# Kernel tuning notes

Measured on AMD Instinct MI355X. Metric: run time of the kernel, lower is better.

The kernel has to match this reference:

```python
import jax, jax.numpy as jnp
import numpy as np

N = 100_000   # num nodes
E = 1_000_000 # num edges
F = 64        # feat_dim
H = 64        # hidden_dim
D = 64        # embed_dim


def _xavier(key, shape):
    limit = float(np.sqrt(6.0 / (shape[0] + shape[1])))
    return jax.random.uniform(key, shape, jnp.float32, -limit, limit)


def setup_inputs() -> dict:
    key = jax.random.key(0)
    ks = jax.random.split(key, 8)
    x = jax.random.normal(ks[0], (N, F), jnp.float32)
    edge_index = jax.random.randint(ks[1], (2, E), 0, N, dtype=jnp.int64)
    # GCNConv weights stored [in, out] (torch Linear transposed); biases zero-init
    return {
        "x": x,
        "edge_index": edge_index,
        "W1": _xavier(ks[2], (F, H)), "b1": jnp.zeros((H,), jnp.float32),
        "W2": _xavier(ks[3], (H, H)), "b2": jnp.zeros((H,), jnp.float32),
        "W3": _xavier(ks[4], (H, D)), "b3": jnp.zeros((D,), jnp.float32),
        "fw1": _xavier(ks[5], (D, H)), "fb1": jnp.zeros((H,), jnp.float32),
        "fw2": _xavier(ks[6], (H, D)), "fb2": jnp.zeros((D,), jnp.float32),
    }


def _gcn_conv(x, src, dst, dinv, W, b):
    # GCNConv: out = D^{-1/2} (A+I) D^{-1/2} (x W) + b
    h = x @ W                                   # [N, out]
    norm = dinv[src] * dinv[dst]                # [E]
    msg = h[src] * norm[:, None]                # gather + scale: [E, out]
    agg = jax.ops.segment_sum(msg, dst, num_segments=N)
    agg = agg + h * (dinv * dinv)[:, None]      # self-loop term
    return agg + b


def reference(x, edge_index, W1, b1, W2, b2, W3, b3, fw1, fb1, fw2, fb2):
    src, dst = edge_index[0], edge_index[1]
    # degree with self-loops (symmetric normalization)
    deg = jax.ops.segment_sum(jnp.ones((E,), x.dtype), dst, num_segments=N) + 1.0
    dinv = jax.lax.rsqrt(deg)
    # eval mode: dropout(p=0.5, training=False) is identity
    h = jax.nn.relu(_gcn_conv(x, src, dst, dinv, W1, b1))
    h = jax.nn.relu(_gcn_conv(h, src, dst, dinv, W2, b2))
    h = jax.nn.relu(_gcn_conv(h, src, dst, dinv, W3, b3))
    h = jax.nn.relu(h @ fw1 + fb1)
    return h @ fw2 + fb2                        # node embeddings [N, D]
```

## Files before the change

### kernel.cpp

```cpp
#include <hip/hip_runtime.h>
#include <cstdint>
#include <cstddef>


#define CDIV(a, b) (((a) + (b) - 1) / (b))

typedef __attribute__((ext_vector_type(8))) short bf16x8;
typedef __attribute__((ext_vector_type(4))) float f32x4;

static constexpr int BKT_SHIFT = 10;
static constexpr int BKT_NODES = 1 << BKT_SHIFT;
static constexpr int BKT_CAP = 13312;

__device__ __forceinline__ void split_bf(float a, short& hi, short& lo) {
  unsigned u = __float_as_uint(a);
  unsigned r = u + (0x7FFF + ((u >> 16) & 1));
  hi = (short)(r >> 16);
  float hirec = __uint_as_float(r & 0xFFFF0000u);
  float res = a - hirec;
  lo = (short)(__float_as_uint(res) >> 16);
}

__device__ __forceinline__ unsigned short f2bf_rne(float a) {
  unsigned u = __float_as_uint(a);
  u += 0x7FFF + ((u >> 16) & 1);
  return (unsigned short)(u >> 16);
}

__device__ __forceinline__ float4 bf4_to_f4(uint2 u) {
  float4 v;
  v.x = __uint_as_float(u.x << 16);
  v.y = __uint_as_float(u.x & 0xFFFF0000u);
  v.z = __uint_as_float(u.y << 16);
  v.w = __uint_as_float(u.y & 0xFFFF0000u);
  return v;
}

__device__ __forceinline__ void split8(float4 x, float4 y, bf16x8& h, bf16x8& l) {
  float av[8] = {x.x, x.y, x.z, x.w, y.x, y.y, y.z, y.w};
#pragma unroll
  for (int j = 0; j < 8; ++j) {
    short hi, lo;
    split_bf(av[j], hi, lo);
    h[j] = hi;
    l[j] = lo;
  }
}

__device__ __forceinline__ float4 nt_ld4(const float* p) {
  f32x4 v = __builtin_nontemporal_load(reinterpret_cast<const f32x4*>(p));
  float4 r;
  r.x = v[0]; r.y = v[1]; r.z = v[2]; r.w = v[3];
  return r;
}

__global__ void k_zero_i32(int* __restrict__ p, int n) {
  int i = blockIdx.x * blockDim.x + threadIdx.x;
  if (i < n) p[i] = 0;
}

__global__ __launch_bounds__(256)
void k_bucket(const int* __restrict__ ei, int* __restrict__ bcnt,
              int2* __restrict__ pairs, int E) {
  __shared__ int hist[128], rbase[128], roff[128];
  int t = threadIdx.x;
  int chunk = (E + gridDim.x - 1) / gridDim.x;
  int e0 = blockIdx.x * chunk;
  int e1 = min(e0 + chunk, E);
  if (t < 128) hist[t] = 0;
  __syncthreads();
  for (int e = e0 + t; e < e1; e += 256) {
    int d = __builtin_nontemporal_load(&ei[E + e]);
    atomicAdd(&hist[d >> BKT_SHIFT], 1);
  }
  __syncthreads();
  if (t < 128) {
    roff[t] = 0;
    rbase[t] = hist[t] ? atomicAdd(&bcnt[t], hist[t]) : 0;
  }
  __syncthreads();
  for (int e = e0 + t; e < e1; e += 256) {
    int d = __builtin_nontemporal_load(&ei[E + e]);
    int s = __builtin_nontemporal_load(&ei[e]);
    int b = d >> BKT_SHIFT;
    int r = atomicAdd(&roff[b], 1);
    int idx = rbase[b] + r;
    if (idx < BKT_CAP) pairs[(size_t)b * BKT_CAP + idx] = make_int2(s, d);
  }
}

__global__ __launch_bounds__(1024)
void k_build(const int2* __restrict__ pairs, const int* __restrict__ bcnt,
             int* __restrict__ row_ptr, float* __restrict__ dinv,
             int* __restrict__ srcs, int N, int E, int K) {
  __shared__ int cnt[BKT_NODES];
  __shared__ int deg[BKT_NODES];
  __shared__ int ebase_sh;
  int b = blockIdx.x;
  int t = threadIdx.x;
  int lo = b << BKT_SHIFT;
  int range = min(BKT_NODES, N - lo);
  int sz = min(bcnt[b], BKT_CAP);
  if (t == 0) {
    int s = 0;
    for (int i = 0; i < b; ++i) s += bcnt[i];
    ebase_sh = s;
  }
  cnt[t] = 0;
  __syncthreads();
  int ebase = ebase_sh;
  const int2* pb = pairs + (size_t)b * BKT_CAP;
  for (int i = t; i < sz; i += 1024) {
    atomicAdd(&cnt[pb[i].y - lo], 1);
  }
  __syncthreads();
  deg[t] = cnt[t];
  __syncthreads();
  int offset = 1;
  for (int d2 = BKT_NODES / 2; d2 > 0; d2 >>= 1) {
    if (t < d2) {
      int ai = offset * (2 * t + 1) - 1;
      int bi = offset * (2 * t + 2) - 1;
      cnt[bi] += cnt[ai];
    }
    offset <<= 1;
    __syncthreads();
  }
  if (t == 0) cnt[BKT_NODES - 1] = 0;
  __syncthreads();
  for (int d2 = 1; d2 < BKT_NODES; d2 <<= 1) {
    offset >>= 1;
    if (t < d2) {
      int ai = offset * (2 * t + 1) - 1;
      int bi = offset * (2 * t + 2) - 1;
      int tmp = cnt[ai];
      cnt[ai] = cnt[bi];
      cnt[bi] += tmp;
    }
    __syncthreads();
  }
  if (t < range) {
    row_ptr[lo + t] = ebase + cnt[t];
    dinv[lo + t] = rsqrtf((float)deg[t] + 1.0f);
  }
  if (b == K - 1 && t == 0) row_ptr[N] = E;
  __syncthreads();
  for (int i = t; i < sz; i += 1024) {
    int2 p = pb[i];
    int pos = ebase + atomicAdd(&cnt[p.y - lo], 1);
    srcs[pos] = p.x;
  }
}

__global__ void k_prep(const float* __restrict__ w0, const float* __restrict__ w1,
                       const float* __restrict__ w2, const float* __restrict__ w3,
                       const float* __restrict__ w4, bf16x8* __restrict__ packed) {
  const float* W;
  switch (blockIdx.x) {
    case 0: W = w0; break;
    case 1: W = w1; break;
    case 2: W = w2; break;
    case 3: W = w3; break;
    default: W = w4; break;
  }
  int tid = threadIdx.x;
  int lane = tid & 63;
  int q = (tid >> 6) & 1;
  int t = tid >> 7;
  int col = lane & 15, quad = lane >> 4;
  bf16x8 hi8, lo8;
#pragma unroll
  for (int j = 0; j < 8; ++j) {
    int k = q * 32 + quad * 8 + j;
    short hi, lo;
    split_bf(W[k * 64 + t * 16 + col], hi, lo);
    hi8[j] = hi;
    lo8[j] = lo;
  }
  size_t base = (size_t)blockIdx.x * 1024 + ((t * 2 + q) * 2) * 64 + lane;
  packed[base] = hi8;
  packed[base + 64] = lo8;
}

__global__ __launch_bounds__(256, 4)
void k_mm(const float* __restrict__ in, const bf16x8* __restrict__ Wp,
          const float* __restrict__ dinv, unsigned short* __restrict__ out, int n) {
  int lane = threadIdx.x & 63;
  int col = lane & 15, quad = lane >> 4;
  int tile = (blockIdx.x * blockDim.x + threadIdx.x) >> 6;
  int ntiles = (n + 15) >> 4;
  if (tile >= ntiles) return;

  bf16x8 wh[4][2], wl[4][2];
#pragma unroll
  for (int t = 0; t < 4; ++t)
#pragma unroll
    for (int q = 0; q < 2; ++q) {
      wh[t][q] = Wp[((t * 2 + q) * 2) * 64 + lane];
      wl[t][q] = Wp[((t * 2 + q) * 2 + 1) * 64 + lane];
    }

  int row0 = tile << 4;
  int ar = row0 + col;
  if (ar > n - 1) ar = n - 1;
  const float* arow = in + (size_t)ar * 64 + quad * 8;
  float4 a0 = nt_ld4(arow), a1 = nt_ld4(arow + 4);
  float4 a2 = nt_ld4(arow + 32), a3 = nt_ld4(arow + 36);

  bf16x8 ah[2], al[2];
  split8(a0, a1, ah[0], al[0]);
  split8(a2, a3, ah[1], al[1]);

  f32x4 acc[4];
#pragma unroll
  for (int t = 0; t < 4; ++t) acc[t] = (f32x4){0.f, 0.f, 0.f, 0.f};
#pragma unroll
  for (int t = 0; t < 4; ++t)
#pragma unroll
    for (int q = 0; q < 2; ++q) {
      acc[t] = __builtin_amdgcn_mfma_f32_16x16x32_bf16(ah[q], wh[t][q], acc[t], 0, 0, 0);
      acc[t] = __builtin_amdgcn_mfma_f32_16x16x32_bf16(ah[q], wl[t][q], acc[t], 0, 0, 0);
      acc[t] = __builtin_amdgcn_mfma_f32_16x16x32_bf16(al[q], wh[t][q], acc[t], 0, 0, 0);
    }
  float dv[4];
#pragma unroll
  for (int r = 0; r < 4; ++r) {
    int row = row0 + quad * 4 + r;
    dv[r] = (row < n) ? dinv[row] : 0.0f;
  }
#pragma unroll
  for (int t = 0; t < 4; ++t)
#pragma unroll
    for (int r = 0; r < 4; ++r) {
      int row = row0 + quad * 4 + r;
      if (row < n) out[(size_t)row * 64 + t * 16 + col] = f2bf_rne(acc[t][r] * dv[r]);
    }
}

template <bool HEAD>
__global__ __launch_bounds__(256, 4)
void k_agg_mm(const unsigned short* __restrict__ hws, const float* __restrict__ dinv,
              const int* __restrict__ row_ptr, const int* __restrict__ srcs,
              const float* __restrict__ bagg,
              const bf16x8* __restrict__ Wp1, const float* __restrict__ b1p,
              const bf16x8* __restrict__ Wp2, const float* __restrict__ b2p,
              void* __restrict__ out, int n) {
  constexpr int LDP = 68;
  __shared__ float a_sh[16 * LDP];
  int tid = threadIdx.x;
  int g = tid >> 4;
  int fg = tid & 15;
  int row0 = blockIdx.x << 4;
  const uint2* hw2 = (const uint2*)hws;

  int node = row0 + g;
  bool valid = node < n;
  int nd = valid ? node : (n - 1);
  uint2 su = hw2[(size_t)nd * 16 + fg];
  int p0 = 0, p1 = 0;
  if (valid) {
    p0 = row_ptr[node];
    p1 = row_ptr[node + 1];
  }
  float4 acc = make_float4(0.f, 0.f, 0.f, 0.f);
  if (p0 < p1) {
    int s[8];
#pragma unroll
    for (int j = 0; j < 8; ++j) {
      int ij = p0 + j;
      ij = (ij < p1) ? ij : (p1 - 1);
      s[j] = __builtin_nontemporal_load(&srcs[ij]);
    }
    for (int p = p0; p < p1; p += 8) {
      uint2 u[8];
#pragma unroll
      for (int j = 0; j < 8; ++j) u[j] = hw2[(size_t)s[j] * 16 + fg];
      int pn = p + 8;
      if (pn < p1) {
#pragma unroll
        for (int j = 0; j < 8; ++j) {
          int ij = pn + j;
          ij = (ij < p1) ? ij : (p1 - 1);
          s[j] = __builtin_nontemporal_load(&srcs[ij]);
        }
      }
      float4 v0 = bf4_to_f4(u[0]);
      acc.x += v0.x;
      acc.y += v0.y;
      acc.z += v0.z;
      acc.w += v0.w;
#pragma unroll
      for (int j = 1; j < 8; ++j) {
        float m = (p + j < p1) ? 1.f : 0.f;
        float4 v = bf4_to_f4(u[j]);
        acc.x = fmaf(m, v.x, acc.x);
        acc.y = fmaf(m, v.y, acc.y);
        acc.z = fmaf(m, v.z, acc.z);
        acc.w = fmaf(m, v.w, acc.w);
      }
    }
  }
  {
    float di = valid ? dinv[node] : 0.f;
    float4 selfv = bf4_to_f4(su);
    float4 b4 = ((const float4*)bagg)[fg];
    float4 r = make_float4(0.f, 0.f, 0.f, 0.f);
    if (valid) {
      r.x = fmaxf(fmaf(di, acc.x + selfv.x, b4.x), 0.f);
      r.y = fmaxf(fmaf(di, acc.y + selfv.y, b4.y), 0.f);
      r.z = fmaxf(fmaf(di, acc.z + selfv.z, b4.z), 0.f);
      r.w = fmaxf(fmaf(di, acc.w + selfv.w, b4.w), 0.f);
    }
    *(float4*)&a_sh[g * LDP + (fg << 2)] = r;
  }
  __syncthreads();

  int lane = threadIdx.x & 63;
  int wave = threadIdx.x >> 6;
  int col = lane & 15, quad = lane >> 4;
  const float* arow = &a_sh[col * LDP + (quad << 3)];
  float4 a0 = *(const float4*)(arow);
  float4 a1 = *(const float4*)(arow + 4);
  float4 a2 = *(const float4*)(arow + 32);
  float4 a3 = *(const float4*)(arow + 36);
  bf16x8 ah[2], al[2];
  split8(a0, a1, ah[0], al[0]);
  split8(a2, a3, ah[1], al[1]);

  bf16x8 wh[2], wl[2];
#pragma unroll
  for (int q = 0; q < 2; ++q) {
    wh[q] = Wp1[((wave * 2 + q) * 2) * 64 + lane];
    wl[q] = Wp1[((wave * 2 + q) * 2 + 1) * 64 + lane];
  }
  f32x4 acc1 = (f32x4){0.f, 0.f, 0.f, 0.f};
#pragma unroll
  for (int q = 0; q < 2; ++q) {
    acc1 = __builtin_amdgcn_mfma_f32_16x16x32_bf16(ah[q], wh[q], acc1, 0, 0, 0);
    acc1 = __builtin_amdgcn_mfma_f32_16x16x32_bf16(ah[q], wl[q], acc1, 0, 0, 0);
    acc1 = __builtin_amdgcn_mfma_f32_16x16x32_bf16(al[q], wh[q], acc1, 0, 0, 0);
  }

  if constexpr (!HEAD) {
#pragma unroll
    for (int r = 0; r < 4; ++r) {
      int row = row0 + (quad << 2) + r;
      if (row < n) {
        ((unsigned short*)out)[(size_t)row * 64 + wave * 16 + col] =
            f2bf_rne(acc1[r] * dinv[row]);
      }
    }
  } else {
    __shared__ float h_sh[16 * LDP];
    float bv1 = b1p[wave * 16 + col];
#pragma unroll
    for (int r = 0; r < 4; ++r) {
      h_sh[((quad << 2) + r) * LDP + wave * 16 + col] = fmaxf(acc1[r] + bv1, 0.f);
    }
    __syncthreads();
    const float* hrow = &h_sh[col * LDP + (quad << 3)];
    float4 h0 = *(const float4*)(hrow);
    float4 h1 = *(const float4*)(hrow + 4);
    float4 h2 = *(const float4*)(hrow + 32);
    float4 h3 = *(const float4*)(hrow + 36);
    bf16x8 ah2[2], al2[2];
    split8(h0, h1, ah2[0], al2[0]);
    split8(h2, h3, ah2[1], al2[1]);
    bf16x8 wh2[2], wl2[2];
#pragma unroll
    for (int q = 0; q < 2; ++q) {
      wh2[q] = Wp2[((wave * 2 + q) * 2) * 64 + lane];
      wl2[q] = Wp2[((wave * 2 + q) * 2 + 1) * 64 + lane];
    }
    f32x4 acc2 = (f32x4){0.f, 0.f, 0.f, 0.f};
#pragma unroll
    for (int q = 0; q < 2; ++q) {
      acc2 = __builtin_amdgcn_mfma_f32_16x16x32_bf16(ah2[q], wh2[q], acc2, 0, 0, 0);
      acc2 = __builtin_amdgcn_mfma_f32_16x16x32_bf16(ah2[q], wl2[q], acc2, 0, 0, 0);
      acc2 = __builtin_amdgcn_mfma_f32_16x16x32_bf16(al2[q], wh2[q], acc2, 0, 0, 0);
    }
    float bv2 = b2p[wave * 16 + col];
#pragma unroll
    for (int r = 0; r < 4; ++r) {
      int row = row0 + (quad << 2) + r;
      if (row < n) {
        ((float*)out)[(size_t)row * 64 + wave * 16 + col] = acc2[r] + bv2;
      }
    }
  }
}

extern "C" void kernel_launch(void* const* d_in, const int* in_sizes, int n_in,
                              void* d_out, int out_size, void* d_ws, size_t ws_size,
                              hipStream_t stream) {
  const float* x = (const float*)d_in[0];
  const int* ei = (const int*)d_in[1];
  const float* W1 = (const float*)d_in[2];
  const float* b1 = (const float*)d_in[3];
  const float* W2 = (const float*)d_in[4];
  const float* b2 = (const float*)d_in[5];
  const float* W3 = (const float*)d_in[6];
  const float* b3 = (const float*)d_in[7];
  const float* fw1 = (const float*)d_in[8];
  const float* fb1 = (const float*)d_in[9];
  const float* fw2 = (const float*)d_in[10];
  const float* fb2 = (const float*)d_in[11];
  float* out = (float*)d_out;

  const int N = in_sizes[0] / 64;
  const int E = in_sizes[1] / 2;
  const int K = CDIV(N, BKT_NODES);

  char* w = (char*)d_ws;
  auto take = [&](size_t bytes) -> char* {
    char* p = w;
    w += (bytes + 255) & ~(size_t)255;
    return p;
  };
  float* dinv = (float*)take((size_t)N * 4);
  int* row_ptr = (int*)take((size_t)(N + 1) * 4);
  int* bcnt = (int*)take((size_t)128 * 4);
  int* srcs = (int*)take((size_t)E * 4);
  bf16x8* wpack = (bf16x8*)take((size_t)5 * 1024 * 16);
  unsigned short* hwsA = (unsigned short*)take((size_t)N * 64 * 2);
  unsigned short* hwsB = (unsigned short*)take((size_t)N * 64 * 2);
  int2* pairs = (int2*)hwsA;

  const int B = 256;

  k_prep<<<5, 512, 0, stream>>>(W1, W2, W3, fw1, fw2, wpack);
  k_zero_i32<<<1, 128, 0, stream>>>(bcnt, 128);
  k_bucket<<<256, B, 0, stream>>>(ei, bcnt, pairs, E);
  k_build<<<K, 1024, 0, stream>>>(pairs, bcnt, row_ptr, dinv, srcs, N, E, K);

  const int ntiles = CDIV(N, 16);
  const int MMG = CDIV(ntiles, 4);

  k_mm<<<MMG, B, 0, stream>>>(x, wpack + 0 * 1024, dinv, hwsA, N);
  k_agg_mm<false><<<ntiles, B, 0, stream>>>(hwsA, dinv, row_ptr, srcs, b1,
                                            wpack + 1 * 1024, nullptr, nullptr, nullptr,
                                            hwsB, N);
  k_agg_mm<false><<<ntiles, B, 0, stream>>>(hwsB, dinv, row_ptr, srcs, b2,
                                            wpack + 2 * 1024, nullptr, nullptr, nullptr,
                                            hwsA, N);
  k_agg_mm<true><<<ntiles, B, 0, stream>>>(hwsA, dinv, row_ptr, srcs, b3,
                                           wpack + 3 * 1024, fb1, wpack + 4 * 1024, fb2,
                                           out, N);
}
```

Baseline: 255.7 us.

## Widen gather to 16B per lane, 32 nodes per block, zero-row padding

The aggregation kernel now uses 8 lanes per node, each loading a 16-byte chunk of 8 bf16 features, and handles 32 nodes per block with two MFMA row tiles. Padded edge slots point at an extra all-zero row N instead of being masked by multiplication. The producing kernels write that zero row. Separately, the bucket-counter zeroing is folded into the weight-prep kernel to drop one launch, and the bucket grid grows to 1024 blocks. The aim is fewer, wider gather loads and less per-edge masking math, at the cost of more registers per thread and extra workspace for the padded row.

Result: slower. 271.2 us (+6.1%).

```diff
diff --git a/kernel.cpp b/kernel.cpp
--- a/kernel.cpp
+++ b/kernel.cpp
@@ -27,15 +27,6 @@
   return (unsigned short)(u >> 16);
 }
 
-__device__ __forceinline__ float4 bf4_to_f4(uint2 u) {
-  float4 v;
-  v.x = __uint_as_float(u.x << 16);
-  v.y = __uint_as_float(u.x & 0xFFFF0000u);
-  v.z = __uint_as_float(u.y << 16);
-  v.w = __uint_as_float(u.y & 0xFFFF0000u);
-  return v;
-}
-
 __device__ __forceinline__ void split8(float4 x, float4 y, bf16x8& h, bf16x8& l) {
   float av[8] = {x.x, x.y, x.z, x.w, y.x, y.y, y.z, y.w};
 #pragma unroll
@@ -52,11 +43,6 @@
   float4 r;
   r.x = v[0]; r.y = v[1]; r.z = v[2]; r.w = v[3];
   return r;
-}
-
-__global__ void k_zero_i32(int* __restrict__ p, int n) {
-  int i = blockIdx.x * blockDim.x + threadIdx.x;
-  if (i < n) p[i] = 0;
 }
 
 __global__ __launch_bounds__(256)
@@ -154,7 +140,12 @@
 
 __global__ void k_prep(const float* __restrict__ w0, const float* __restrict__ w1,
                        const float* __restrict__ w2, const float* __restrict__ w3,
-                       const float* __restrict__ w4, bf16x8* __restrict__ packed) {
+                       const float* __restrict__ w4, bf16x8* __restrict__ packed,
+                       int* __restrict__ bcnt) {
+  if (blockIdx.x == 5) {
+    if (threadIdx.x < 128) bcnt[threadIdx.x] = 0;
+    return;
+  }
   const float* W;
   switch (blockIdx.x) {
     case 0: W = w0; break;
@@ -185,6 +176,9 @@
 __global__ __launch_bounds__(256, 4)
 void k_mm(const float* __restrict__ in, const bf16x8* __restrict__ Wp,
           const float* __restrict__ dinv, unsigned short* __restrict__ out, int n) {
+  if (blockIdx.x == 0 && threadIdx.x < 32) {
+    ((unsigned int*)out)[(size_t)n * 32 + threadIdx.x] = 0u;
+  }
   int lane = threadIdx.x & 63;
   int col = lane & 15, quad = lane >> 4;
   int tile = (blockIdx.x * blockDim.x + threadIdx.x) >> 6;
@@ -246,86 +240,89 @@
               const bf16x8* __restrict__ Wp2, const float* __restrict__ b2p,
               void* __restrict__ out, int n) {
   constexpr int LDP = 68;
-  __shared__ float a_sh[16 * LDP];
+  __shared__ float a_sh[32 * LDP];
   int tid = threadIdx.x;
-  int g = tid >> 4;
-  int fg = tid & 15;
-  int row0 = blockIdx.x << 4;
-  const uint2* hw2 = (const uint2*)hws;
+  int g = tid >> 3;
+  int fg = tid & 7;
+  int row0 = blockIdx.x << 5;
+  const uint4* hw4 = (const uint4*)hws;
+
+  if (!HEAD && blockIdx.x == 0 && tid < 32) {
+    ((unsigned int*)out)[(size_t)n * 32 + tid] = 0u;
+  }
 
   int node = row0 + g;
   bool valid = node < n;
-  int nd = valid ? node : (n - 1);
-  uint2 su = hw2[(size_t)nd * 16 + fg];
+  int nd = valid ? node : n;
+  uint4 su = hw4[(size_t)nd * 8 + fg];
+  float di = valid ? dinv[node] : 0.f;
   int p0 = 0, p1 = 0;
   if (valid) {
     p0 = row_ptr[node];
     p1 = row_ptr[node + 1];
   }
-  float4 acc = make_float4(0.f, 0.f, 0.f, 0.f);
+  float acc[8] = {0.f, 0.f, 0.f, 0.f, 0.f, 0.f, 0.f, 0.f};
   if (p0 < p1) {
     int s[8];
 #pragma unroll
     for (int j = 0; j < 8; ++j) {
       int ij = p0 + j;
-      ij = (ij < p1) ? ij : (p1 - 1);
-      s[j] = __builtin_nontemporal_load(&srcs[ij]);
+      bool ok = ij < p1;
+      int sv = __builtin_nontemporal_load(&srcs[ok ? ij : p1 - 1]);
+      s[j] = ok ? sv : n;
     }
     for (int p = p0; p < p1; p += 8) {
-      uint2 u[8];
-#pragma unroll
-      for (int j = 0; j < 8; ++j) u[j] = hw2[(size_t)s[j] * 16 + fg];
+      uint4 u[8];
+#pragma unroll
+      for (int j = 0; j < 8; ++j) u[j] = hw4[(size_t)s[j] * 8 + fg];
       int pn = p + 8;
       if (pn < p1) {
 #pragma unroll
         for (int j = 0; j < 8; ++j) {
           int ij = pn + j;
-          ij = (ij < p1) ? ij : (p1 - 1);
-          s[j] = __builtin_nontemporal_load(&srcs[ij]);
+          bool ok = ij < p1;
+          int sv = __builtin_nontemporal_load(&srcs[ok ? ij : p1 - 1]);
+          s[j] = ok ? sv : n;
         }
       }
-      float4 v0 = bf4_to_f4(u[0]);
-      acc.x += v0.x;
-      acc.y += v0.y;
-      acc.z += v0.z;
-      acc.w += v0.w;
-#pragma unroll
-      for (int j = 1; j < 8; ++j) {
-        float m = (p + j < p1) ? 1.f : 0.f;
-        float4 v = bf4_to_f4(u[j]);
-        acc.x = fmaf(m, v.x, acc.x);
-        acc.y = fmaf(m, v.y, acc.y);
-        acc.z = fmaf(m, v.z, acc.z);
-        acc.w = fmaf(m, v.w, acc.w);
+#pragma unroll
+      for (int j = 0; j < 8; ++j) {
+        acc[0] += __uint_as_float(u[j].x << 16);
+        acc[1] += __uint_as_float(u[j].x & 0xFFFF0000u);
+        acc[2] += __uint_as_float(u[j].y << 16);
+        acc[3] += __uint_as_float(u[j].y & 0xFFFF0000u);
+        acc[4] += __uint_as_float(u[j].z << 16);
+        acc[5] += __uint_as_float(u[j].z & 0xFFFF0000u);
+        acc[6] += __uint_as_float(u[j].w << 16);
+        acc[7] += __uint_as_float(u[j].w & 0xFFFF0000u);
       }
     }
   }
   {
-    float di = valid ? dinv[node] : 0.f;
-    float4 selfv = bf4_to_f4(su);
-    float4 b4 = ((const float4*)bagg)[fg];
-    float4 r = make_float4(0.f, 0.f, 0.f, 0.f);
-    if (valid) {
-      r.x = fmaxf(fmaf(di, acc.x + selfv.x, b4.x), 0.f);
-      r.y = fmaxf(fmaf(di, acc.y + selfv.y, b4.y), 0.f);
-      r.z = fmaxf(fmaf(di, acc.z + selfv.z, b4.z), 0.f);
-      r.w = fmaxf(fmaf(di, acc.w + selfv.w, b4.w), 0.f);
-    }
-    *(float4*)&a_sh[g * LDP + (fg << 2)] = r;
-  }
-  __syncthreads();
-
-  int lane = threadIdx.x & 63;
-  int wave = threadIdx.x >> 6;
+    float sf[8];
+    sf[0] = __uint_as_float(su.x << 16);
+    sf[1] = __uint_as_float(su.x & 0xFFFF0000u);
+    sf[2] = __uint_as_float(su.y << 16);
+    sf[3] = __uint_as_float(su.y & 0xFFFF0000u);
+    sf[4] = __uint_as_float(su.z << 16);
+    sf[5] = __uint_as_float(su.z & 0xFFFF0000u);
+    sf[6] = __uint_as_float(su.w << 16);
+    sf[7] = __uint_as_float(su.w & 0xFFFF0000u);
+    float r[8];
+#pragma unroll
+    for (int k = 0; k < 8; ++k) {
+      float bk = bagg[fg * 8 + k];
+      r[k] = valid ? fmaxf(fmaf(di, acc[k] + sf[k], bk), 0.f) : 0.f;
+    }
+    float* dst = &a_sh[g * LDP + (fg << 3)];
+    *(float4*)(dst) = make_float4(r[0], r[1], r[2], r[3]);
+    *(float4*)(dst + 4) = make_float4(r[4], r[5], r[6], r[7]);
+  }
+  __syncthreads();
+
+  int lane = tid & 63;
+  int wave = tid >> 6;
   int col = lane & 15, quad = lane >> 4;
-  const float* arow = &a_sh[col * LDP + (quad << 3)];
-  float4 a0 = *(const float4*)(arow);
-  float4 a1 = *(const float4*)(arow + 4);
-  float4 a2 = *(const float4*)(arow + 32);
-  float4 a3 = *(const float4*)(arow + 36);
-  bf16x8 ah[2], al[2];
-  split8(a0, a1, ah[0], al[0]);
-  split8(a2, a3, ah[1], al[1]);
 
   bf16x8 wh[2], wl[2];
 #pragma unroll
@@ -333,58 +330,78 @@
     wh[q] = Wp1[((wave * 2 + q) * 2) * 64 + lane];
     wl[q] = Wp1[((wave * 2 + q) * 2 + 1) * 64 + lane];
   }
-  f32x4 acc1 = (f32x4){0.f, 0.f, 0.f, 0.f};
-#pragma unroll
-  for (int q = 0; q < 2; ++q) {
-    acc1 = __builtin_amdgcn_mfma_f32_16x16x32_bf16(ah[q], wh[q], acc1, 0, 0, 0);
-    acc1 = __builtin_amdgcn_mfma_f32_16x16x32_bf16(ah[q], wl[q], acc1, 0, 0, 0);
-    acc1 = __builtin_amdgcn_mfma_f32_16x16x32_bf16(al[q], wh[q], acc1, 0, 0, 0);
+  f32x4 acc1[2];
+#pragma unroll
+  for (int rt = 0; rt < 2; ++rt) {
+    const float* arow = &a_sh[(rt * 16 + col) * LDP + (quad << 3)];
+    float4 a0 = *(const float4*)(arow);
+    float4 a1 = *(const float4*)(arow + 4);
+    float4 a2 = *(const float4*)(arow + 32);
+    float4 a3 = *(const float4*)(arow + 36);
+    bf16x8 ah[2], al[2];
+    split8(a0, a1, ah[0], al[0]);
+    split8(a2, a3, ah[1], al[1]);
+    acc1[rt] = (f32x4){0.f, 0.f, 0.f, 0.f};
+#pragma unroll
+    for (int q = 0; q < 2; ++q) {
+      acc1[rt] = __builtin_amdgcn_mfma_f32_16x16x32_bf16(ah[q], wh[q], acc1[rt], 0, 0, 0);
+      acc1[rt] = __builtin_amdgcn_mfma_f32_16x16x32_bf16(ah[q], wl[q], acc1[rt], 0, 0, 0);
+      acc1[rt] = __builtin_amdgcn_mfma_f32_16x16x32_bf16(al[q], wh[q], acc1[rt], 0, 0, 0);
+    }
   }
 
   if constexpr (!HEAD) {
 #pragma unroll
-    for (int r = 0; r < 4; ++r) {
-      int row = row0 + (quad << 2) + r;
-      if (row < n) {
-        ((unsigned short*)out)[(size_t)row * 64 + wave * 16 + col] =
-            f2bf_rne(acc1[r] * dinv[row]);
-      }
-    }
+    for (int rt = 0; rt < 2; ++rt)
+#pragma unroll
+      for (int r = 0; r < 4; ++r) {
+        int row = row0 + rt * 16 + (quad << 2) + r;
+        if (row < n) {
+          ((unsigned short*)out)[(size_t)row * 64 + wave * 16 + col] =
+              f2bf_rne(acc1[rt][r] * dinv[row]);
+        }
+      }
   } else {
-    __shared__ float h_sh[16 * LDP];
+    __shared__ float h_sh[32 * LDP];
     float bv1 = b1p[wave * 16 + col];
 #pragma unroll
-    for (int r = 0; r < 4; ++r) {
-      h_sh[((quad << 2) + r) * LDP + wave * 16 + col] = fmaxf(acc1[r] + bv1, 0.f);
-    }
+    for (int rt = 0; rt < 2; ++rt)
+#pragma unroll
+      for (int r = 0; r < 4; ++r) {
+        h_sh[(rt * 16 + (quad << 2) + r) * LDP + wave * 16 + col] =
+            fmaxf(acc1[rt][r] + bv1, 0.f);
+      }
     __syncthreads();
-    const float* hrow = &h_sh[col * LDP + (quad << 3)];
-    float4 h0 = *(const float4*)(hrow);
-    float4 h1 = *(const float4*)(hrow + 4);
-    float4 h2 = *(const float4*)(hrow + 32);
-    float4 h3 = *(const float4*)(hrow + 36);
-    bf16x8 ah2[2], al2[2];
-    split8(h0, h1, ah2[0], al2[0]);
-    split8(h2, h3, ah2[1], al2[1]);
     bf16x8 wh2[2], wl2[2];
 #pragma unroll
     for (int q = 0; q < 2; ++q) {
       wh2[q] = Wp2[((wave * 2 + q) * 2) * 64 + lane];
       wl2[q] = Wp2[((wave * 2 + q) * 2 + 1) * 64 + lane];
     }
-    f32x4 acc2 = (f32x4){0.f, 0.f, 0.f, 0.f};
-#pragma unroll
-    for (int q = 0; q < 2; ++q) {
-      acc2 = __builtin_amdgcn_mfma_f32_16x16x32_bf16(ah2[q], wh2[q], acc2, 0, 0, 0);
-      acc2 = __builtin_amdgcn_mfma_f32_16x16x32_bf16(ah2[q], wl2[q], acc2, 0, 0, 0);
-      acc2 = __builtin_amdgcn_mfma_f32_16x16x32_bf16(al2[q], wh2[q], acc2, 0, 0, 0);
-    }
     float bv2 = b2p[wave * 16 + col];
 #pragma unroll
-    for (int r = 0; r < 4; ++r) {
-      int row = row0 + (quad << 2) + r;
-      if (row < n) {
-        ((float*)out)[(size_t)row * 64 + wave * 16 + col] = acc2[r] + bv2;
+    for (int rt = 0; rt < 2; ++rt) {
+      const float* hrow = &h_sh[(rt * 16 + col) * LDP + (quad << 3)];
+      float4 h0 = *(const float4*)(hrow);
+      float4 h1 = *(const float4*)(hrow + 4);
+      float4 h2 = *(const float4*)(hrow + 32);
+      float4 h3 = *(const float4*)(hrow + 36);
+      bf16x8 ah2[2], al2[2];
+      split8(h0, h1, ah2[0], al2[0]);
+      split8(h2, h3, ah2[1], al2[1]);
+      f32x4 acc2 = (f32x4){0.f, 0.f, 0.f, 0.f};
+#pragma unroll
+      for (int q = 0; q < 2; ++q) {
+        acc2 = __builtin_amdgcn_mfma_f32_16x16x32_bf16(ah2[q], wh2[q], acc2, 0, 0, 0);
+        acc2 = __builtin_amdgcn_mfma_f32_16x16x32_bf16(ah2[q], wl2[q], acc2, 0, 0, 0);
+        acc2 = __builtin_amdgcn_mfma_f32_16x16x32_bf16(al2[q], wh2[q], acc2, 0, 0, 0);
+      }
+#pragma unroll
+      for (int r = 0; r < 4; ++r) {
+        int row = row0 + rt * 16 + (quad << 2) + r;
+        if (row < n) {
+          ((float*)out)[(size_t)row * 64 + wave * 16 + col] = acc2[r] + bv2;
+        }
       }
     }
   }
@@ -422,28 +439,28 @@
   int* bcnt = (int*)take((size_t)128 * 4);
   int* srcs = (int*)take((size_t)E * 4);
   bf16x8* wpack = (bf16x8*)take((size_t)5 * 1024 * 16);
-  unsigned short* hwsA = (unsigned short*)take((size_t)N * 64 * 2);
-  unsigned short* hwsB = (unsigned short*)take((size_t)N * 64 * 2);
+  unsigned short* hwsA = (unsigned short*)take((size_t)(N + 1) * 64 * 2);
+  unsigned short* hwsB = (unsigned short*)take((size_t)(N + 1) * 64 * 2);
   int2* pairs = (int2*)hwsA;
 
   const int B = 256;
 
-  k_prep<<<5, 512, 0, stream>>>(W1, W2, W3, fw1, fw2, wpack);
-  k_zero_i32<<<1, 128, 0, stream>>>(bcnt, 128);
-  k_bucket<<<256, B, 0, stream>>>(ei, bcnt, pairs, E);
+  k_prep<<<6, 512, 0, stream>>>(W1, W2, W3, fw1, fw2, wpack, bcnt);
+  k_bucket<<<1024, B, 0, stream>>>(ei, bcnt, pairs, E);
   k_build<<<K, 1024, 0, stream>>>(pairs, bcnt, row_ptr, dinv, srcs, N, E, K);
 
-  const int ntiles = CDIV(N, 16);
-  const int MMG = CDIV(ntiles, 4);
+  const int ntiles16 = CDIV(N, 16);
+  const int MMG = CDIV(ntiles16, 4);
+  const int ntiles32 = CDIV(N, 32);
 
   k_mm<<<MMG, B, 0, stream>>>(x, wpack + 0 * 1024, dinv, hwsA, N);
-  k_agg_mm<false><<<ntiles, B, 0, stream>>>(hwsA, dinv, row_ptr, srcs, b1,
-                                            wpack + 1 * 1024, nullptr, nullptr, nullptr,
-                                            hwsB, N);
-  k_agg_mm<false><<<ntiles, B, 0, stream>>>(hwsB, dinv, row_ptr, srcs, b2,
-                                            wpack + 2 * 1024, nullptr, nullptr, nullptr,
-                                            hwsA, N);
-  k_agg_mm<true><<<ntiles, B, 0, stream>>>(hwsA, dinv, row_ptr, srcs, b3,
-                                           wpack + 3 * 1024, fb1, wpack + 4 * 1024, fb2,
-                                           out, N);
-}
+  k_agg_mm<false><<<ntiles32, B, 0, stream>>>(hwsA, dinv, row_ptr, srcs, b1,
+                                              wpack + 1 * 1024, nullptr, nullptr, nullptr,
+                                              hwsB, N);
+  k_agg_mm<false><<<ntiles32, B, 0, stream>>>(hwsB, dinv, row_ptr, srcs, b2,
+                                              wpack + 2 * 1024, nullptr, nullptr, nullptr,
+                                              hwsA, N);
+  k_agg_mm<true><<<ntiles32, B, 0, stream>>>(hwsA, dinv, row_ptr, srcs, b3,
+                                             wpack + 3 * 1024, fb1, wpack + 4 * 1024, fb2,
+                                             out, N);
+}
```
